# Kernel tuning notes

Measured on AMD Instinct MI355X. Metric: run time of the kernel, lower is better.

Reference implementation:

```python
import jax, jax.numpy as jnp
import numpy as np

N_NODES = 50000
N_EDGES = 1600000
F = 64
EPS = 1e-05


def setup_inputs() -> dict:
    key = jax.random.key(0)
    k1, k2 = jax.random.split(key)
    e = jax.random.normal(k1, (N_EDGES, F), dtype=jnp.float32)
    dst = jax.random.randint(k2, (N_EDGES,), 0, N_NODES, dtype=jnp.int32)
    gamma = jnp.ones((F,), dtype=jnp.float32)
    beta = jnp.zeros((F,), dtype=jnp.float32)
    return {"e": e, "gamma": gamma, "beta": beta, "dst": dst}


def reference(e, gamma, beta, dst):
    # Per-destination-node statistics over the mailbox [deg, F]:
    #   mean over all deg*F elements; std is torch.std -> unbiased (n-1).
    f = e.shape[1]
    ones = jnp.ones((e.shape[0],), dtype=e.dtype)
    deg = jax.ops.segment_sum(ones, dst, num_segments=N_NODES)          # [N]
    cnt = deg * f                                                        # elements per node
    s = jax.ops.segment_sum(e.sum(axis=-1), dst, num_segments=N_NODES)  # [N]
    ss = jax.ops.segment_sum((e * e).sum(axis=-1), dst, num_segments=N_NODES)
    safe_cnt = jnp.maximum(cnt, 1.0)
    mean = s / safe_cnt
    var = (ss - cnt * mean * mean) / jnp.maximum(cnt - 1.0, 1.0)  # unbiased
    std = jnp.sqrt(jnp.maximum(var, 0.0))
    # Broadcast dst stats back per edge and normalize: (e - mean) / (std + eps)
    norm_e = (e - mean[dst][:, None]) / (std[dst][:, None] + EPS)
    return gamma * norm_e + beta
```

## Files before the change

### kernel.cpp

```cpp
#include <hip/hip_runtime.h>

#define N_NODES_C 50000
#define FDIM 64
#define EPS_C 1e-5f

#define PARTS 16
#define NPP 3125
#define SLICE (3 * NPP)
#define BPERP 64
#define SCAT_BLK 512
#define SCAT_GRID (PARTS * BPERP)

#define EDGE_ACC(D, SV, QV)                                            \
    { unsigned l_ = (unsigned)((D) - lo);                              \
      if (l_ < NPP) { atomicAdd(&sm[l_], (SV));                        \
                      atomicAdd(&sm[NPP + l_], (QV));                  \
                      atomicAdd(&sm[2 * NPP + l_], 1.0f); } }

__global__ void __launch_bounds__(256)
partial_kernel(const float4* __restrict__ e4, float2* __restrict__ partials,
               int nEdges) {
    const int total = nEdges * 16;
    const int stride = gridDim.x * blockDim.x;
    for (int idx = blockIdx.x * blockDim.x + threadIdx.x; idx < total; idx += stride) {
        float4 v = e4[idx];
        float sum = (v.x + v.y) + (v.z + v.w);
        float sq  = (v.x * v.x + v.y * v.y) + (v.z * v.z + v.w * v.w);
#pragma unroll
        for (int m = 1; m < 16; m <<= 1) {
            sum += __shfl_xor(sum, m);
            sq  += __shfl_xor(sq,  m);
        }
        if ((idx & 15) == 0) partials[idx >> 4] = make_float2(sum, sq);
    }
}

__global__ void __launch_bounds__(SCAT_BLK, 8)
scatter_kernel(const int* __restrict__ dst, const float2* __restrict__ partials,
               float* __restrict__ acc, int nEdges) {
    __shared__ float sm[SLICE];
    const int tid = threadIdx.x;
    for (int i = tid; i < SLICE; i += SCAT_BLK) sm[i] = 0.0f;
    __syncthreads();

    const int p  = blockIdx.x / BPERP;
    const int b  = blockIdx.x % BPERP;
    const int lo = p * NPP;

    const int step = BPERP * SCAT_BLK * 8;
    for (int i0 = (b * SCAT_BLK + tid) * 8; i0 < nEdges; i0 += step) {
        if (i0 + 7 < nEdges) {
            int4   da = *(const int4*)(dst + i0);
            int4   db = *(const int4*)(dst + i0 + 4);
            float4 p0 = *(const float4*)(partials + i0);
            float4 p1 = *(const float4*)(partials + i0 + 2);
            float4 p2 = *(const float4*)(partials + i0 + 4);
            float4 p3 = *(const float4*)(partials + i0 + 6);
            EDGE_ACC(da.x, p0.x, p0.y); EDGE_ACC(da.y, p0.z, p0.w);
            EDGE_ACC(da.z, p1.x, p1.y); EDGE_ACC(da.w, p1.z, p1.w);
            EDGE_ACC(db.x, p2.x, p2.y); EDGE_ACC(db.y, p2.z, p2.w);
            EDGE_ACC(db.z, p3.x, p3.y); EDGE_ACC(db.w, p3.z, p3.w);
        } else {
            for (int i = i0; i < nEdges; ++i) {
                float2 pq = partials[i];
                EDGE_ACC(dst[i], pq.x, pq.y);
            }
        }
    }
    __syncthreads();
    float* __restrict__ outp = acc + (size_t)blockIdx.x * SLICE;
    for (int i = tid; i < SLICE; i += SCAT_BLK) outp[i] = sm[i];
}

__global__ void __launch_bounds__(256)
reduce_finalize_kernel(const float* __restrict__ acc, float2* __restrict__ stats,
                       int nNodes) {
    int n = blockIdx.x * blockDim.x + threadIdx.x;
    if (n >= nNodes) return;
    int p = n / NPP, local = n - p * NPP;
    const float* bptr = acc + (size_t)(p * BPERP) * SLICE + local;
    float s = 0.f, q = 0.f, dg = 0.f;
#pragma unroll 8
    for (int bb = 0; bb < BPERP; ++bb, bptr += SLICE) {
        s  += bptr[0];
        q  += bptr[NPP];
        dg += bptr[2 * NPP];
    }
    float cnt  = dg * (float)FDIM;
    float safe = fmaxf(cnt, 1.0f);
    float mean = s / safe;
    float var  = (q - cnt * mean * mean) / fmaxf(cnt - 1.0f, 1.0f);
    float stdv = sqrtf(fmaxf(var, 0.0f));
    stats[n] = make_float2(mean, 1.0f / (stdv + EPS_C));
}

__global__ void __launch_bounds__(256)
norm_kernel(const float4* __restrict__ e4, const int* __restrict__ dst,
            const float2* __restrict__ stats,
            const float4* __restrict__ gamma4, const float4* __restrict__ beta4,
            float4* __restrict__ out4, int nEdges) {
    const int total  = nEdges * 16;
    const int stride = gridDim.x * blockDim.x;
    const int gtid   = blockIdx.x * blockDim.x + threadIdx.x;
    const int sub    = gtid & 15;
    const float4 g = gamma4[sub];
    const float4 b = beta4[sub];
    const int nIter = (total + stride - 1) / stride;
    for (int it = nIter - 1; it >= 0; --it) {
        int idx = it * stride + gtid;
        if (idx >= total) continue;
        float2 mi = stats[dst[idx >> 4]];
        float4 v  = e4[idx];
        float4 o;
        o.x = g.x * (v.x - mi.x) * mi.y + b.x;
        o.y = g.y * (v.y - mi.x) * mi.y + b.y;
        o.z = g.z * (v.z - mi.x) * mi.y + b.z;
        o.w = g.w * (v.w - mi.x) * mi.y + b.w;
        out4[idx] = o;
    }
}

extern "C" void kernel_launch(void* const* d_in, const int* in_sizes, int n_in,
                              void* d_out, int out_size, void* d_ws, size_t ws_size,
                              hipStream_t stream) {
    const float* e     = (const float*)d_in[0];
    const float* gamma = (const float*)d_in[1];
    const float* beta  = (const float*)d_in[2];
    const int*   dst   = (const int*)d_in[3];
    const int nEdges = in_sizes[3];
    const int nNodes = N_NODES_C;

    float*  acc      = (float*)d_ws;
    float2* stats    = (float2*)(acc + (size_t)SCAT_GRID * SLICE);
    float2* partials = stats + nNodes;

    partial_kernel<<<2048, 256, 0, stream>>>((const float4*)e, partials, nEdges);
    scatter_kernel<<<SCAT_GRID, SCAT_BLK, 0, stream>>>(dst, partials, acc, nEdges);
    reduce_finalize_kernel<<<(nNodes + 255) / 256, 256, 0, stream>>>(acc, stats, nNodes);
    norm_kernel<<<2048, 256, 0, stream>>>(
        (const float4*)e, dst, stats,
        (const float4*)gamma, (const float4*)beta,
        (float4*)d_out, nEdges);
}
```

Baseline: 270.8 us.

## Use nontemporal stores and retune scatter blocks per partition and per-thread edge batch

```diff
diff --git a/kernel.cpp b/kernel.cpp
--- a/kernel.cpp
+++ b/kernel.cpp
@@ -7,9 +7,16 @@
 #define PARTS 16
 #define NPP 3125
 #define SLICE (3 * NPP)
-#define BPERP 64
+#define BPERP 48
 #define SCAT_BLK 512
 #define SCAT_GRID (PARTS * BPERP)
+
+typedef float vfloat4 __attribute__((ext_vector_type(4)));
+
+__device__ __forceinline__ void nt_store_f4(float4* p, float x, float y, float z, float w) {
+    vfloat4 v = { x, y, z, w };
+    __builtin_nontemporal_store(v, (vfloat4*)p);
+}
 
 #define EDGE_ACC(D, SV, QV)                                            \
     { unsigned l_ = (unsigned)((D) - lo);                              \
@@ -31,11 +38,16 @@
             sum += __shfl_xor(sum, m);
             sq  += __shfl_xor(sq,  m);
         }
-        if ((idx & 15) == 0) partials[idx >> 4] = make_float2(sum, sq);
+        if ((idx & 15) == 0) {
+            unsigned long long bits;
+            float2 pq = make_float2(sum, sq);
+            __builtin_memcpy(&bits, &pq, 8);
+            __builtin_nontemporal_store(bits, (unsigned long long*)(partials + (idx >> 4)));
+        }
     }
 }
 
-__global__ void __launch_bounds__(SCAT_BLK, 8)
+__global__ void __launch_bounds__(SCAT_BLK, 6)
 scatter_kernel(const int* __restrict__ dst, const float2* __restrict__ partials,
                float* __restrict__ acc, int nEdges) {
     __shared__ float sm[SLICE];
@@ -47,19 +59,14 @@
     const int b  = blockIdx.x % BPERP;
     const int lo = p * NPP;
 
-    const int step = BPERP * SCAT_BLK * 8;
-    for (int i0 = (b * SCAT_BLK + tid) * 8; i0 < nEdges; i0 += step) {
-        if (i0 + 7 < nEdges) {
-            int4   da = *(const int4*)(dst + i0);
-            int4   db = *(const int4*)(dst + i0 + 4);
-            float4 p0 = *(const float4*)(partials + i0);
-            float4 p1 = *(const float4*)(partials + i0 + 2);
-            float4 p2 = *(const float4*)(partials + i0 + 4);
-            float4 p3 = *(const float4*)(partials + i0 + 6);
-            EDGE_ACC(da.x, p0.x, p0.y); EDGE_ACC(da.y, p0.z, p0.w);
-            EDGE_ACC(da.z, p1.x, p1.y); EDGE_ACC(da.w, p1.z, p1.w);
-            EDGE_ACC(db.x, p2.x, p2.y); EDGE_ACC(db.y, p2.z, p2.w);
-            EDGE_ACC(db.z, p3.x, p3.y); EDGE_ACC(db.w, p3.z, p3.w);
+    const int step = BPERP * SCAT_BLK * 4;
+    for (int i0 = (b * SCAT_BLK + tid) * 4; i0 < nEdges; i0 += step) {
+        if (i0 + 3 < nEdges) {
+            int4   d4  = *(const int4*)(dst + i0);
+            float4 p01 = *(const float4*)(partials + i0);
+            float4 p23 = *(const float4*)(partials + i0 + 2);
+            EDGE_ACC(d4.x, p01.x, p01.y); EDGE_ACC(d4.y, p01.z, p01.w);
+            EDGE_ACC(d4.z, p23.x, p23.y); EDGE_ACC(d4.w, p23.z, p23.w);
         } else {
             for (int i = i0; i < nEdges; ++i) {
                 float2 pq = partials[i];
@@ -69,7 +76,9 @@
     }
     __syncthreads();
     float* __restrict__ outp = acc + (size_t)blockIdx.x * SLICE;
-    for (int i = tid; i < SLICE; i += SCAT_BLK) outp[i] = sm[i];
+    for (int i = tid; i < SLICE; i += SCAT_BLK) {
+        __builtin_nontemporal_store(sm[i], outp + i);
+    }
 }
 
 __global__ void __launch_bounds__(256)
@@ -111,12 +120,11 @@
         if (idx >= total) continue;
         float2 mi = stats[dst[idx >> 4]];
         float4 v  = e4[idx];
-        float4 o;
-        o.x = g.x * (v.x - mi.x) * mi.y + b.x;
-        o.y = g.y * (v.y - mi.x) * mi.y + b.y;
-        o.z = g.z * (v.z - mi.x) * mi.y + b.z;
-        o.w = g.w * (v.w - mi.x) * mi.y + b.w;
-        out4[idx] = o;
+        nt_store_f4(out4 + idx,
+                    g.x * (v.x - mi.x) * mi.y + b.x,
+                    g.y * (v.y - mi.x) * mi.y + b.y,
+                    g.z * (v.z - mi.x) * mi.y + b.z,
+                    g.w * (v.w - mi.x) * mi.y + b.w);
     }
 }
 
```

After: 246.9 us, median of 2. 8.8% less time.
